# Performance work log

Measured on AMD Instinct MI355X. Metric: run time of the kernel, lower is better.

## Reference

```python
import jax, jax.numpy as jnp
import numpy as np

N = 50000      # number of graph nodes
D = 128        # in_dim == out_dim
R = 4          # num_ring
NNZ = 800000   # edges per ring (avg degree 16)


def setup_inputs() -> dict:
    key = jax.random.key(0)
    ks = jax.random.split(key, 12)
    s = 1.0 / np.sqrt(D)
    x = jax.random.normal(ks[0], (N, D), jnp.float32)
    W_self = jax.random.normal(ks[1], (D, D), jnp.float32) * s
    W_rings = jax.random.normal(ks[2], (R, D, D), jnp.float32) * s
    WC = jax.random.normal(ks[3], (D, D), jnp.float32) * s
    WD = jax.random.normal(ks[4], (D, D), jnp.float32) * s
    att_w = jax.random.normal(ks[5], (1, 2 * (R + 1) * D), jnp.float32) * s
    att_b = jnp.zeros((1,), jnp.float32)
    # degree^-0.5 style norms: positive, in (0, 1]
    out_deg_norm = jax.random.uniform(ks[6], (N, 1), jnp.float32, 0.05, 1.0)
    in_deg_norm = jax.random.uniform(ks[7], (N, 1), jnp.float32, 0.05, 1.0)
    rows = jax.random.randint(ks[8], (R, NNZ), 0, N, jnp.int32)
    cols = jax.random.randint(ks[9], (R, NNZ), 0, N, jnp.int32)
    return {"x": x, "W_self": W_self, "W_rings": W_rings, "WC": WC, "WD": WD,
            "att_w": att_w, "att_b": att_b, "out_deg_norm": out_deg_norm,
            "in_deg_norm": in_deg_norm, "rows": rows, "cols": cols}


def reference(x, W_self, W_rings, WC, WD, att_w, att_b, out_deg_norm, in_deg_norm, rows, cols):
    n, d = x.shape
    r = W_rings.shape[0]
    # ---- ring-wise sparse aggregation (dropout is identity at inference) ----
    z_self = x @ W_self.T                       # [N, D]
    z_list = [z_self]
    for i in range(r):
        h = (x @ W_rings[i].T) * out_deg_norm   # [N, D]
        # torch.sparse.mm(adj, h): out[row] += h[col] for each edge (row, col)
        z_i = jax.ops.segment_sum(h[cols[i]], rows[i], num_segments=n)
        z_list.append(z_i)
    z = jnp.concatenate(z_list, axis=1) * in_deg_norm   # [N, (R+1)*D]
    # ---- heterogeneous sensitivity interaction ----
    z3 = z.reshape(n, r + 1, d)                          # [N, R+1, D]
    z_hat_com = z3 @ WC                                  # [N, R+1, D]
    com_score = jnp.einsum('nrd,nsd->nrs', z_hat_com, z_hat_com)
    alpha_com = jax.nn.softmax(com_score, axis=-1)
    z_com = jnp.einsum('nrs,nsd->nrd', alpha_com, z_hat_com).reshape(n, -1)
    z_hat_dis = z3 @ WD                                  # [N, R+1, D]
    # pairwise differences: sub[n, r, s, :] = zd[n, r] - zd[n, s]
    sub = z_hat_dis[:, :, None, :] - z_hat_dis[:, None, :, :]   # [N, R+1, R+1, D]
    dis_score = jnp.einsum('nrd,nrsd->nrs', z_hat_dis, sub)
    alpha_dis = jax.nn.softmax(dis_score, axis=-1)
    z_dis = jnp.einsum('nrs,nrsd->nrd', alpha_dis, sub).reshape(n, -1)
    z_cat = jnp.concatenate([z_com, z_dis], axis=-1)     # [N, 2*(R+1)*D]
    beta = jax.nn.sigmoid(z_cat @ att_w.T + att_b)       # [N, 1]
    z_wave = beta * z_com + (1.0 - beta) * z_dis         # [N, (R+1)*D]
    return z_wave
```

## Files before the change

### kernel.cpp

```cpp
#include <hip/hip_runtime.h>
#include <hip/hip_bf16.h>

#define NN 50000
#define D 128
#define RR 4
#define NNZ 800000
#define NCHUNK 196

typedef float v2f    __attribute__((ext_vector_type(2)));
typedef float f32x4  __attribute__((ext_vector_type(4)));
typedef short bf16x8 __attribute__((ext_vector_type(8)));

static __device__ __forceinline__ unsigned short f2b(float f)
{
    __hip_bfloat16 h = __float2bfloat16(f);
    return *reinterpret_cast<unsigned short*>(&h);
}
static __device__ __forceinline__ float b2f(unsigned short u)
{
    union { unsigned u32; float f; } v; v.u32 = ((unsigned)u) << 16; return v.f;
}

__global__ __launch_bounds__(256) void hist_kernel(
    const int* __restrict__ rows, int* __restrict__ cnt)
{
    const int r = blockIdx.y;
    const int e = blockIdx.x * 256 + threadIdx.x;
    atomicAdd(&cnt[r * NN + rows[(size_t)r * NNZ + e]], 1);
}

__global__ __launch_bounds__(256) void scanA_kernel(
    const int* __restrict__ cnt, int* __restrict__ bsum)
{
    const int r = blockIdx.y, bx = blockIdx.x, t = threadIdx.x;
    const int idx = bx * 256 + t;
    int v = (idx < NN) ? cnt[r * NN + idx] : 0;
#pragma unroll
    for (int off = 32; off; off >>= 1) v += __shfl_xor(v, off);
    __shared__ int ws4[4];
    if ((t & 63) == 0) ws4[t >> 6] = v;
    __syncthreads();
    if (t == 0) bsum[r * NCHUNK + bx] = ws4[0] + ws4[1] + ws4[2] + ws4[3];
}

__global__ __launch_bounds__(256) void scanB_kernel(int* __restrict__ bsum)
{
    __shared__ int s[256];
    const int t = threadIdx.x;
    for (int r = 0; r < RR; ++r) {
        int v = (t < NCHUNK) ? bsum[r * NCHUNK + t] : 0;
        s[t] = v;
        __syncthreads();
        for (int off = 1; off < 256; off <<= 1) {
            int u = (t >= off) ? s[t - off] : 0;
            __syncthreads();
            s[t] += u;
            __syncthreads();
        }
        if (t < NCHUNK) bsum[r * NCHUNK + t] = s[t] - v;
        __syncthreads();
    }
}

__global__ __launch_bounds__(256) void scanC_kernel(
    const int* __restrict__ cnt, const int* __restrict__ bsum,
    int* __restrict__ rowptr, int* __restrict__ cursor)
{
    const int r = blockIdx.y, bx = blockIdx.x, t = threadIdx.x;
    const int idx = bx * 256 + t;
    int v = (idx < NN) ? cnt[r * NN + idx] : 0;
    __shared__ int s[256];
    s[t] = v;
    __syncthreads();
    for (int off = 1; off < 256; off <<= 1) {
        int u = (t >= off) ? s[t - off] : 0;
        __syncthreads();
        s[t] += u;
        __syncthreads();
    }
    const int excl = bsum[r * NCHUNK + bx] + s[t] - v;
    if (idx <= NN) rowptr[r * (NN + 1) + idx] = excl;
    if (idx < NN)  cursor[r * NN + idx] = excl;
}

__global__ __launch_bounds__(256) void fill_kernel(
    const int* __restrict__ rows, const int* __restrict__ cols,
    int* __restrict__ cursor, int* __restrict__ perm)
{
    const int r = blockIdx.y;
    const int e = blockIdx.x * 256 + threadIdx.x;
    const int row = rows[(size_t)r * NNZ + e];
    const int pos = atomicAdd(&cursor[r * NN + row], 1);
    perm[(size_t)r * NNZ + pos] = cols[(size_t)r * NNZ + e];
}

__global__ __launch_bounds__(256) void convw_kernel(
    const float* __restrict__ Wself, const float* __restrict__ Wrings,
    unsigned short* __restrict__ wh, unsigned short* __restrict__ wl)
{
    int idx = blockIdx.x * 256 + threadIdx.x;
    int jg = idx >> 7, k = idx & 127;
    float f = (jg < 128) ? Wself[(size_t)jg * 128 + k]
                         : Wrings[(size_t)(jg - 128) * 128 + k];
    unsigned short hi = f2b(f);
    wh[idx] = hi;
    wl[idx] = f2b(f - b2f(hi));
}

__global__ __launch_bounds__(256) void convt_kernel(
    const float* __restrict__ WC, const float* __restrict__ WD,
    unsigned short* __restrict__ wct_h, unsigned short* __restrict__ wct_l,
    unsigned short* __restrict__ wdt_h, unsigned short* __restrict__ wdt_l)
{
    int idx = blockIdx.x * 256 + threadIdx.x;
    int kk = idx >> 7, col = idx & 127;
    float c = WC[idx];
    float d = WD[idx];
    unsigned short ch = f2b(c), dh = f2b(d);
    wct_h[col * 128 + kk] = ch;
    wct_l[col * 128 + kk] = f2b(c - b2f(ch));
    wdt_h[col * 128 + kk] = dh;
    wdt_l[col * 128 + kk] = f2b(d - b2f(dh));
}

__global__ __launch_bounds__(256) void gather2_kernel(
    const float* __restrict__ x, const float* __restrict__ odn,
    const int* __restrict__ rp, const int* __restrict__ pm,
    float* __restrict__ y, int r0)
{
    const int cr = blockIdx.y + r0;
    const int t = threadIdx.x;
    const int row = blockIdx.x * 4 + (t >> 6);
    const int l  = t & 63;
    const int h  = l >> 5;
    const int dq = l & 31;
    const int* rpr = rp + (size_t)cr * (NN + 1);
    const int s = rpr[row], e = rpr[row + 1];
    const int* pmr = pm + (size_t)cr * NNZ;

    f32x4 acc = {0.f, 0.f, 0.f, 0.f};
    int i = s;
    for (; i + 8 <= e; i += 8) {
        int c0 = pmr[i + h],     c1 = pmr[i + 2 + h];
        int c2 = pmr[i + 4 + h], c3 = pmr[i + 6 + h];
        float o0 = odn[c0], o1 = odn[c1], o2 = odn[c2], o3 = odn[c3];
        f32x4 v0 = *(const f32x4*)&x[(size_t)c0 * D + dq * 4];
        f32x4 v1 = *(const f32x4*)&x[(size_t)c1 * D + dq * 4];
        f32x4 v2 = *(const f32x4*)&x[(size_t)c2 * D + dq * 4];
        f32x4 v3 = *(const f32x4*)&x[(size_t)c3 * D + dq * 4];
        acc += v0 * o0 + v1 * o1 + v2 * o2 + v3 * o3;
    }
    for (; i + h < e; i += 2) {
        int c = pmr[i + h];
        acc += (*(const f32x4*)&x[(size_t)c * D + dq * 4]) * odn[c];
    }
#pragma unroll
    for (int j = 0; j < 4; ++j) acc[j] += __shfl_xor(acc[j], 32);
    if (h == 0)
        *(f32x4*)&y[((size_t)blockIdx.y * NN + row) * D + dq * 4] = acc;
}

__global__ __launch_bounds__(256) void gemm5_kernel(
    const float* __restrict__ x, const float* __restrict__ y,
    const unsigned short* __restrict__ wh, const unsigned short* __restrict__ wl,
    float* __restrict__ out, int s0, int r0)
{
    const int s = s0 + blockIdx.y;
    const float* A = (s == 0) ? x : y + (size_t)(s - 1 - r0) * NN * D;
    const int t = threadIdx.x;
    const int w = t >> 6, l = t & 63;
    const int lr = l & 15, lk = l >> 4;
    const int n0 = blockIdx.x * 16;

    bf16x8 ah[4], al[4];
    const float* xr = A + (size_t)(n0 + lr) * D + lk * 8;
#pragma unroll
    for (int ks = 0; ks < 4; ++ks) {
        float4 v0 = *(const float4*)(xr + ks * 32);
        float4 v1 = *(const float4*)(xr + ks * 32 + 4);
        float f[8] = {v0.x, v0.y, v0.z, v0.w, v1.x, v1.y, v1.z, v1.w};
#pragma unroll
        for (int j = 0; j < 8; ++j) {
            unsigned short hi = f2b(f[j]);
            ah[ks][j] = (short)hi;
            al[ks][j] = (short)f2b(f[j] - b2f(hi));
        }
    }

#pragma unroll
    for (int j = 0; j < 2; ++j) {
        const int ctl = w + 4 * j;
        const int jg  = s * 128 + ctl * 16 + lr;
        f32x4 acc = {0.f, 0.f, 0.f, 0.f};
#pragma unroll
        for (int ks = 0; ks < 4; ++ks) {
            bf16x8 bhv = *(const bf16x8*)&wh[(size_t)jg * D + ks * 32 + lk * 8];
            bf16x8 blv = *(const bf16x8*)&wl[(size_t)jg * D + ks * 32 + lk * 8];
            acc = __builtin_amdgcn_mfma_f32_16x16x32_bf16(ah[ks], bhv, acc, 0, 0, 0);
            acc = __builtin_amdgcn_mfma_f32_16x16x32_bf16(al[ks], bhv, acc, 0, 0, 0);
            acc = __builtin_amdgcn_mfma_f32_16x16x32_bf16(ah[ks], blv, acc, 0, 0, 0);
        }
#pragma unroll
        for (int q = 0; q < 4; ++q) {
            int n = n0 + lk * 4 + q;
            out[(size_t)n * 640 + jg] = acc[q];
        }
    }
}

__device__ __forceinline__ int sidx(int r, int s)
{
    if (r > s) { int t = r; r = s; s = t; }
    return r * 5 + s - (r * (r + 1)) / 2;
}

__global__ __launch_bounds__(512, 4) void interact2_kernel(
    float* __restrict__ z,
    const unsigned short* __restrict__ wct_h, const unsigned short* __restrict__ wct_l,
    const unsigned short* __restrict__ wdt_h, const unsigned short* __restrict__ wdt_l,
    const float* __restrict__ att_w, const float* __restrict__ att_b,
    const float* __restrict__ idn)
{
    __shared__ float SB[2 * 5 * 16 * 128];

    const int t  = threadIdx.x;
    const int w  = t >> 6;
    const int l  = t & 63;
    const int lr = l & 15;
    const int lk = l >> 4;
    const int n0 = blockIdx.x * 16;

    const int mm = w >> 2;
    const int nq = w & 3;
    const unsigned short* bhp = mm ? wdt_h : wct_h;
    const unsigned short* blp = mm ? wdt_l : wct_l;

    f32x4 acc[5][2];
#pragma unroll
    for (int mt = 0; mt < 5; ++mt) {
        acc[mt][0] = (f32x4){0.f, 0.f, 0.f, 0.f};
        acc[mt][1] = (f32x4){0.f, 0.f, 0.f, 0.f};
    }

#pragma unroll
    for (int mt = 0; mt < 5; ++mt) {
        bf16x8 ah[4], al[4];
        const float* ap = z + (size_t)(n0 + lr) * 640 + mt * 128 + lk * 8;
#pragma unroll
        for (int ks = 0; ks < 4; ++ks) {
            float4 v0 = *(const float4*)(ap + ks * 32);
            float4 v1 = *(const float4*)(ap + ks * 32 + 4);
            float f[8] = {v0.x, v0.y, v0.z, v0.w, v1.x, v1.y, v1.z, v1.w};
#pragma unroll
            for (int j = 0; j < 8; ++j) {
                unsigned short hi = f2b(f[j]);
                ah[ks][j] = (short)hi;
                al[ks][j] = (short)f2b(f[j] - b2f(hi));
            }
        }
#pragma unroll
        for (int nt = 0; nt < 2; ++nt) {
            const int col = nq * 32 + nt * 16 + lr;
#pragma unroll
            for (int ks = 0; ks < 4; ++ks) {
                bf16x8 vh = *(const bf16x8*)&bhp[(size_t)col * 128 + ks * 32 + lk * 8];
                bf16x8 vl = *(const bf16x8*)&blp[(size_t)col * 128 + ks * 32 + lk * 8];
                acc[mt][nt] = __builtin_amdgcn_mfma_f32_16x16x32_bf16(ah[ks], vh, acc[mt][nt], 0, 0, 0);
                acc[mt][nt] = __builtin_amdgcn_mfma_f32_16x16x32_bf16(al[ks], vh, acc[mt][nt], 0, 0, 0);
                acc[mt][nt] = __builtin_amdgcn_mfma_f32_16x16x32_bf16(ah[ks], vl, acc[mt][nt], 0, 0, 0);
            }
        }
    }

#pragma unroll
    for (int mt = 0; mt < 5; ++mt)
#pragma unroll
        for (int nt = 0; nt < 2; ++nt) {
            const int col = nq * 32 + nt * 16 + lr;
#pragma unroll
            for (int q = 0; q < 4; ++q) {
                const int nd = lk * 4 + q;
                SB[(((mm * 5 + mt) * 16) + nd) * 128 + col] = acc[mt][nt][q];
            }
        }
    __syncthreads();

#pragma unroll
    for (int ii = 0; ii < 2; ++ii) {
        const int nd = w + ii * 8;
        const int n  = n0 + nd;
        const float nf = idn[n];

        v2f ar[5], dr[5];
#pragma unroll
        for (int r = 0; r < 5; ++r) {
            ar[r] = *(const v2f*)&SB[((r * 16) + nd) * 128 + 2 * l] * nf;
            dr[r] = *(const v2f*)&SB[(((5 + r) * 16) + nd) * 128 + 2 * l] * nf;
        }

        float pc[15], pd[15];
        {
            int k = 0;
#pragma unroll
            for (int r = 0; r < 5; ++r)
#pragma unroll
                for (int s = r; s < 5; ++s, ++k) {
                    v2f qc = ar[r] * ar[s];
                    v2f qd = dr[r] * dr[s];
                    float vc = qc.x + qc.y;
                    float vd = qd.x + qd.y;
#pragma unroll
                    for (int off = 32; off; off >>= 1) {
                        vc += __shfl_xor(vc, off);
                        vd += __shfl_xor(vd, off);
                    }
                    pc[k] = vc; pd[k] = vd;
                }
        }

        v2f zcom[5], zdis[5];
#pragma unroll
        for (int r = 0; r < 5; ++r) {
            float sc[5], m = -1e30f;
#pragma unroll
            for (int s = 0; s < 5; ++s) { sc[s] = pc[sidx(r, s)]; m = fmaxf(m, sc[s]); }
            float e[5], se = 0.f;
#pragma unroll
            for (int s = 0; s < 5; ++s) { e[s] = __expf(sc[s] - m); se += e[s]; }
            float inv = 1.f / se;
            v2f a2 = (v2f)0.f;
#pragma unroll
            for (int s = 0; s < 5; ++s) a2 += ar[s] * e[s];
            zcom[r] = a2 * inv;

            float qq = pd[sidx(r, r)];
            float sd[5], md = -1e30f;
#pragma unroll
            for (int s = 0; s < 5; ++s) { sd[s] = qq - pd[sidx(r, s)]; md = fmaxf(md, sd[s]); }
            float ed[5], sed = 0.f;
#pragma unroll
            for (int s = 0; s < 5; ++s) { ed[s] = __expf(sd[s] - md); sed += ed[s]; }
            float invd = 1.f / sed;
            v2f d2 = (v2f)0.f;
#pragma unroll
            for (int s = 0; s < 5; ++s) d2 += dr[s] * ed[s];
            zdis[r] = dr[r] - d2 * invd;
        }

        v2f p2 = (v2f)0.f;
#pragma unroll
        for (int r = 0; r < 5; ++r) {
            p2 += (*(const v2f*)&att_w[r * 128 + 2 * l]) * zcom[r];
            p2 += (*(const v2f*)&att_w[640 + r * 128 + 2 * l]) * zdis[r];
        }
        float part = p2.x + p2.y;
#pragma unroll
        for (int off = 32; off; off >>= 1) part += __shfl_xor(part, off);
        const float beta = 1.f / (1.f + __expf(-(part + att_b[0])));
        const float omb  = 1.f - beta;

#pragma unroll
        for (int r = 0; r < 5; ++r) {
            v2f o = zcom[r] * beta + zdis[r] * omb;
            *(v2f*)&z[(size_t)n * 640 + r * 128 + 2 * l] = o;
        }
    }
}

extern "C" void kernel_launch(void* const* d_in, const int* in_sizes, int n_in,
                              void* d_out, int out_size, void* d_ws, size_t ws_size,
                              hipStream_t stream)
{
    const float* x      = (const float*)d_in[0];
    const float* W_self = (const float*)d_in[1];
    const float* W_ring = (const float*)d_in[2];
    const float* WC     = (const float*)d_in[3];
    const float* WD     = (const float*)d_in[4];
    const float* att_w  = (const float*)d_in[5];
    const float* att_b  = (const float*)d_in[6];
    const float* odn    = (const float*)d_in[7];
    const float* idn    = (const float*)d_in[8];
    const int*   rows   = (const int*)d_in[9];
    const int*   cols   = (const int*)d_in[10];
    float* out = (float*)d_out;

    const size_t wb_sz  = (size_t)640 * 128 * 2;
    const size_t wt_sz  = (size_t)128 * 128 * 2;
    const size_t y1_sz  = (size_t)NN * D * 4;
    const size_t cnt_sz = (size_t)RR * NN * 4;
    const size_t rp_sz  = (size_t)RR * (NN + 1) * 4;
    const size_t cur_sz = (size_t)RR * NN * 4;
    const size_t bs_sz  = 4096;
    const size_t pm_sz  = (size_t)RR * NNZ * 4;
    const size_t fixed  = 2 * wb_sz + 4 * wt_sz + cnt_sz + rp_sz + cur_sz + bs_sz + pm_sz;
    const bool big = ws_size >= fixed + RR * y1_sz + 4096;

    char* p = (char*)d_ws;
    unsigned short* wh    = (unsigned short*)p; p += wb_sz;
    unsigned short* wl    = (unsigned short*)p; p += wb_sz;
    unsigned short* wct_h = (unsigned short*)p; p += wt_sz;
    unsigned short* wct_l = (unsigned short*)p; p += wt_sz;
    unsigned short* wdt_h = (unsigned short*)p; p += wt_sz;
    unsigned short* wdt_l = (unsigned short*)p; p += wt_sz;
    float* y    = (float*)p; p += (big ? RR : 1) * y1_sz;
    int* cnt    = (int*)p; p += cnt_sz;
    int* rowptr = (int*)p; p += rp_sz;
    int* cursor = (int*)p; p += cur_sz;
    int* bsum   = (int*)p; p += bs_sz;
    int* perm   = (int*)p;

    convw_kernel<<<320, 256, 0, stream>>>(W_self, W_ring, wh, wl);
    convt_kernel<<<64, 256, 0, stream>>>(WC, WD, wct_h, wct_l, wdt_h, wdt_l);

    hipMemsetAsync(cnt, 0, cnt_sz, stream);
    hist_kernel<<<dim3(NNZ / 256, RR), 256, 0, stream>>>(rows, cnt);
    scanA_kernel<<<dim3(NCHUNK, RR), 256, 0, stream>>>(cnt, bsum);
    scanB_kernel<<<1, 256, 0, stream>>>(bsum);
    scanC_kernel<<<dim3(NCHUNK, RR), 256, 0, stream>>>(cnt, bsum, rowptr, cursor);
    fill_kernel<<<dim3(NNZ / 256, RR), 256, 0, stream>>>(rows, cols, cursor, perm);

    if (big) {
        gather2_kernel<<<dim3(NN / 4, RR), 256, 0, stream>>>(x, odn, rowptr, perm, y, 0);
        gemm5_kernel<<<dim3(NN / 16, 5), 256, 0, stream>>>(x, y, wh, wl, out, 0, 0);
    } else {
        gemm5_kernel<<<dim3(NN / 16, 1), 256, 0, stream>>>(x, y, wh, wl, out, 0, 0);
        for (int r = 0; r < RR; ++r) {
            gather2_kernel<<<dim3(NN / 4, 1), 256, 0, stream>>>(x, odn, rowptr, perm, y, r);
            gemm5_kernel<<<dim3(NN / 16, 1), 256, 0, stream>>>(x, y, wh, wl, out, r + 1, r);
        }
    }

    interact2_kernel<<<NN / 16, 512, 0, stream>>>(out, wct_h, wct_l, wdt_h, wdt_l,
                                                  att_w, att_b, idn);
}
```

Baseline: 1.176 ms.

## Fuse per-ring projection GEMM with interaction kernel to skip z round-trip

In the big-workspace path, the 5-way projection GEMM and the interaction kernel are merged into one kernel. Each block computes its 16 nodes' z tile in registers, stages it as bf16 hi/lo in an 80KB LDS buffer, runs the WC/WD GEMMs and the softmax interaction from LDS, and writes only the final output. This removes writing and re-reading the N×640 fp32 intermediate and one kernel launch. In exchange, the large LDS footprint with 512 threads may limit occupancy, and the z values are re-split into bf16 hi/lo pairs rather than read from fp32.

```diff
diff --git a/kernel.cpp b/kernel.cpp
--- a/kernel.cpp
+++ b/kernel.cpp
@@ -212,6 +212,223 @@
 {
     if (r > s) { int t = r; r = s; s = t; }
     return r * 5 + s - (r * (r + 1)) / 2;
+}
+
+__global__ __launch_bounds__(512, 4) void fused_kernel(
+    const float* __restrict__ x, const float* __restrict__ y,
+    const unsigned short* __restrict__ wh, const unsigned short* __restrict__ wl,
+    const unsigned short* __restrict__ wct_h, const unsigned short* __restrict__ wct_l,
+    const unsigned short* __restrict__ wdt_h, const unsigned short* __restrict__ wdt_l,
+    const float* __restrict__ att_w, const float* __restrict__ att_b,
+    const float* __restrict__ idn, float* __restrict__ out)
+{
+    __shared__ __align__(16) char LB[81920];
+
+    const int t  = threadIdx.x;
+    const int w  = t >> 6;
+    const int l  = t & 63;
+    const int lr = l & 15;
+    const int lk = l >> 4;
+    const int n0 = blockIdx.x * 16;
+
+#pragma unroll
+    for (int i = 0; i < 5; ++i) {
+        const int fi = i * 512 + t;
+        const int e  = fi * 4;
+        const int s  = e >> 11;
+        const int nd = (e >> 7) & 15;
+        const int k0 = e & 127;
+        const float* src = (s == 0)
+            ? &x[(size_t)(n0 + nd) * 128 + k0]
+            : &y[((size_t)(s - 1) * NN + (n0 + nd)) * 128 + k0];
+        f32x4 v = *(const f32x4*)src;
+        const int row  = s * 16 + nd;
+        const int boff = ((row * 128 + k0) * 2) ^ ((row & 7) << 4);
+        ushort4 hv, lv;
+        unsigned short h0 = f2b(v[0]), h1 = f2b(v[1]), h2 = f2b(v[2]), h3 = f2b(v[3]);
+        hv.x = h0; hv.y = h1; hv.z = h2; hv.w = h3;
+        lv.x = f2b(v[0] - b2f(h0)); lv.y = f2b(v[1] - b2f(h1));
+        lv.z = f2b(v[2] - b2f(h2)); lv.w = f2b(v[3] - b2f(h3));
+        *(ushort4*)(LB + boff)         = hv;
+        *(ushort4*)(LB + 20480 + boff) = lv;
+    }
+    __syncthreads();
+
+    f32x4 zacc[5];
+#pragma unroll
+    for (int j = 0; j < 5; ++j) zacc[j] = (f32x4){0.f, 0.f, 0.f, 0.f};
+
+#pragma unroll
+    for (int j = 0; j < 5; ++j) {
+        const int jg = (w + 8 * j) * 16 + lr;
+#pragma unroll
+        for (int ks = 0; ks < 4; ++ks) {
+            const int arow  = j * 16 + lr;
+            const int abyte = ((arow * 128 + ks * 32 + lk * 8) * 2) ^ ((arow & 7) << 4);
+            bf16x8 ah = *(const bf16x8*)(LB + abyte);
+            bf16x8 al = *(const bf16x8*)(LB + 20480 + abyte);
+            bf16x8 bh = *(const bf16x8*)&wh[(size_t)jg * 128 + ks * 32 + lk * 8];
+            bf16x8 bl = *(const bf16x8*)&wl[(size_t)jg * 128 + ks * 32 + lk * 8];
+            zacc[j] = __builtin_amdgcn_mfma_f32_16x16x32_bf16(ah, bh, zacc[j], 0, 0, 0);
+            zacc[j] = __builtin_amdgcn_mfma_f32_16x16x32_bf16(al, bh, zacc[j], 0, 0, 0);
+            zacc[j] = __builtin_amdgcn_mfma_f32_16x16x32_bf16(ah, bl, zacc[j], 0, 0, 0);
+        }
+    }
+    __syncthreads();
+
+    {
+        const int k = w * 16 + lr;
+#pragma unroll
+        for (int j = 0; j < 5; ++j)
+#pragma unroll
+            for (int q = 0; q < 4; ++q) {
+                const int nd  = lk * 4 + q;
+                const int row = j * 16 + nd;
+                const float zv = zacc[j][q];
+                const unsigned short hi = f2b(zv);
+                const unsigned short lo = f2b(zv - b2f(hi));
+                const int boff = ((row * 128 + k) * 2) ^ ((row & 7) << 4);
+                *(unsigned short*)(LB + boff)         = hi;
+                *(unsigned short*)(LB + 20480 + boff) = lo;
+            }
+    }
+    __syncthreads();
+
+    const int mm = w >> 2;
+    const int nq = w & 3;
+    const unsigned short* bhp = mm ? wdt_h : wct_h;
+    const unsigned short* blp = mm ? wdt_l : wct_l;
+
+    f32x4 acc2[5][2];
+#pragma unroll
+    for (int mt = 0; mt < 5; ++mt) {
+        acc2[mt][0] = (f32x4){0.f, 0.f, 0.f, 0.f};
+        acc2[mt][1] = (f32x4){0.f, 0.f, 0.f, 0.f};
+    }
+
+#pragma unroll
+    for (int ks = 0; ks < 4; ++ks) {
+        const int c0 = nq * 32 + lr;
+        const int c1 = c0 + 16;
+        bf16x8 bh0 = *(const bf16x8*)&bhp[(size_t)c0 * 128 + ks * 32 + lk * 8];
+        bf16x8 bl0 = *(const bf16x8*)&blp[(size_t)c0 * 128 + ks * 32 + lk * 8];
+        bf16x8 bh1 = *(const bf16x8*)&bhp[(size_t)c1 * 128 + ks * 32 + lk * 8];
+        bf16x8 bl1 = *(const bf16x8*)&blp[(size_t)c1 * 128 + ks * 32 + lk * 8];
+#pragma unroll
+        for (int mt = 0; mt < 5; ++mt) {
+            const int arow  = mt * 16 + lr;
+            const int abyte = ((arow * 128 + ks * 32 + lk * 8) * 2) ^ ((arow & 7) << 4);
+            bf16x8 zh = *(const bf16x8*)(LB + abyte);
+            bf16x8 zl = *(const bf16x8*)(LB + 20480 + abyte);
+            acc2[mt][0] = __builtin_amdgcn_mfma_f32_16x16x32_bf16(zh, bh0, acc2[mt][0], 0, 0, 0);
+            acc2[mt][0] = __builtin_amdgcn_mfma_f32_16x16x32_bf16(zl, bh0, acc2[mt][0], 0, 0, 0);
+            acc2[mt][0] = __builtin_amdgcn_mfma_f32_16x16x32_bf16(zh, bl0, acc2[mt][0], 0, 0, 0);
+            acc2[mt][1] = __builtin_amdgcn_mfma_f32_16x16x32_bf16(zh, bh1, acc2[mt][1], 0, 0, 0);
+            acc2[mt][1] = __builtin_amdgcn_mfma_f32_16x16x32_bf16(zl, bh1, acc2[mt][1], 0, 0, 0);
+            acc2[mt][1] = __builtin_amdgcn_mfma_f32_16x16x32_bf16(zh, bl1, acc2[mt][1], 0, 0, 0);
+        }
+    }
+    __syncthreads();
+
+#pragma unroll
+    for (int mt = 0; mt < 5; ++mt)
+#pragma unroll
+        for (int nt = 0; nt < 2; ++nt) {
+            const int col = nq * 32 + nt * 16 + lr;
+#pragma unroll
+            for (int q = 0; q < 4; ++q) {
+                const int nd  = lk * 4 + q;
+                const int row = (mm * 5 + mt) * 16 + nd;
+                const int boff = (row * 512 + col * 4) ^ (((row >> 2) & 3) << 4);
+                *(float*)(LB + boff) = acc2[mt][nt][q];
+            }
+        }
+    __syncthreads();
+
+#pragma unroll
+    for (int ii = 0; ii < 2; ++ii) {
+        const int nd = w + ii * 8;
+        const int n  = n0 + nd;
+        const float nf = idn[n];
+
+        v2f ar[5], dr[5];
+#pragma unroll
+        for (int r = 0; r < 5; ++r) {
+            const int rowc = r * 16 + nd;
+            const int rowd = (5 + r) * 16 + nd;
+            const int bc = (rowc * 512 + l * 8) ^ (((rowc >> 2) & 3) << 4);
+            const int bd = (rowd * 512 + l * 8) ^ (((rowd >> 2) & 3) << 4);
+            ar[r] = *(const v2f*)(LB + bc) * nf;
+            dr[r] = *(const v2f*)(LB + bd) * nf;
+        }
+
+        float pc[15], pd[15];
+        {
+            int k = 0;
+#pragma unroll
+            for (int r = 0; r < 5; ++r)
+#pragma unroll
+                for (int s = r; s < 5; ++s, ++k) {
+                    v2f qc = ar[r] * ar[s];
+                    v2f qd = dr[r] * dr[s];
+                    float vc = qc.x + qc.y;
+                    float vd = qd.x + qd.y;
+#pragma unroll
+                    for (int off = 32; off; off >>= 1) {
+                        vc += __shfl_xor(vc, off);
+                        vd += __shfl_xor(vd, off);
+                    }
+                    pc[k] = vc; pd[k] = vd;
+                }
+        }
+
+        v2f zcom[5], zdis[5];
+#pragma unroll
+        for (int r = 0; r < 5; ++r) {
+            float sc[5], m = -1e30f;
+#pragma unroll
+            for (int s = 0; s < 5; ++s) { sc[s] = pc[sidx(r, s)]; m = fmaxf(m, sc[s]); }
+            float e[5], se = 0.f;
+#pragma unroll
+            for (int s = 0; s < 5; ++s) { e[s] = __expf(sc[s] - m); se += e[s]; }
+            float inv = 1.f / se;
+            v2f a2 = (v2f)0.f;
+#pragma unroll
+            for (int s = 0; s < 5; ++s) a2 += ar[s] * e[s];
+            zcom[r] = a2 * inv;
+
+            float qq = pd[sidx(r, r)];
+            float sd[5], md = -1e30f;
+#pragma unroll
+            for (int s = 0; s < 5; ++s) { sd[s] = qq - pd[sidx(r, s)]; md = fmaxf(md, sd[s]); }
+            float ed[5], sed = 0.f;
+#pragma unroll
+            for (int s = 0; s < 5; ++s) { ed[s] = __expf(sd[s] - md); sed += ed[s]; }
+            float invd = 1.f / sed;
+            v2f d2 = (v2f)0.f;
+#pragma unroll
+            for (int s = 0; s < 5; ++s) d2 += dr[s] * ed[s];
+            zdis[r] = dr[r] - d2 * invd;
+        }
+
+        v2f p2 = (v2f)0.f;
+#pragma unroll
+        for (int r = 0; r < 5; ++r) {
+            p2 += (*(const v2f*)&att_w[r * 128 + 2 * l]) * zcom[r];
+            p2 += (*(const v2f*)&att_w[640 + r * 128 + 2 * l]) * zdis[r];
+        }
+        float part = p2.x + p2.y;
+#pragma unroll
+        for (int off = 32; off; off >>= 1) part += __shfl_xor(part, off);
+        const float beta = 1.f / (1.f + __expf(-(part + att_b[0])));
+        const float omb  = 1.f - beta;
+
+#pragma unroll
+        for (int r = 0; r < 5; ++r) {
+            v2f o = zcom[r] * beta + zdis[r] * omb;
+            *(v2f*)&out[(size_t)n * 640 + r * 128 + 2 * l] = o;
+        }
+    }
 }
 
 __global__ __launch_bounds__(512, 4) void interact2_kernel(
@@ -421,15 +638,16 @@
 
     if (big) {
         gather2_kernel<<<dim3(NN / 4, RR), 256, 0, stream>>>(x, odn, rowptr, perm, y, 0);
-        gemm5_kernel<<<dim3(NN / 16, 5), 256, 0, stream>>>(x, y, wh, wl, out, 0, 0);
+        fused_kernel<<<NN / 16, 512, 0, stream>>>(x, y, wh, wl,
+                                                  wct_h, wct_l, wdt_h, wdt_l,
+                                                  att_w, att_b, idn, out);
     } else {
         gemm5_kernel<<<dim3(NN / 16, 1), 256, 0, stream>>>(x, y, wh, wl, out, 0, 0);
         for (int r = 0; r < RR; ++r) {
             gather2_kernel<<<dim3(NN / 4, 1), 256, 0, stream>>>(x, odn, rowptr, perm, y, r);
             gemm5_kernel<<<dim3(NN / 16, 1), 256, 0, stream>>>(x, y, wh, wl, out, r + 1, r);
         }
-    }
-
-    interact2_kernel<<<NN / 16, 512, 0, stream>>>(out, wct_h, wct_l, wdt_h, wdt_l,
-                                                  att_w, att_b, idn);
-}
+        interact2_kernel<<<NN / 16, 512, 0, stream>>>(out, wct_h, wct_l, wdt_h, wdt_l,
+                                                      att_w, att_b, idn);
+    }
+}
```

New measurement: 1.008 ms. 1.17x faster.

## Fold ring weights into WC/WD and fuse projection with interaction kernel

Applied to the files above, without the earlier changes.

Precomputes combined weight products (W_s^T·WC and W_s^T·WD) once, so the per-node pipeline does a single GEMM from the raw x and aggregated inputs straight into the com/dis projections. This removes the intermediate [N,640] z write/read and the separate gemm5 pass. Inputs are pre-split into bf16 hi/lo halves in global memory, the reductions use DPP/swizzle instead of shuffles, and shared memory gets an XOR swizzle. The fused kernel now does 10 matrix products per node tile and needs more workspace. The low-memory fallback path is dropped, and the reassociated weight product changes rounding slightly.

```diff
diff --git a/kernel.cpp b/kernel.cpp
--- a/kernel.cpp
+++ b/kernel.cpp
@@ -19,6 +19,21 @@
 static __device__ __forceinline__ float b2f(unsigned short u)
 {
     union { unsigned u32; float f; } v; v.u32 = ((unsigned)u) << 16; return v.f;
+}
+
+static __device__ __forceinline__ float redux32(float v)
+{
+    int i;
+    i = __builtin_amdgcn_update_dpp(0, __float_as_int(v), 0xB1, 0xF, 0xF, true);
+    v += __int_as_float(i);
+    i = __builtin_amdgcn_update_dpp(0, __float_as_int(v), 0x4E, 0xF, 0xF, true);
+    v += __int_as_float(i);
+    i = __builtin_amdgcn_update_dpp(0, __float_as_int(v), 0x141, 0xF, 0xF, true);
+    v += __int_as_float(i);
+    i = __builtin_amdgcn_update_dpp(0, __float_as_int(v), 0x140, 0xF, 0xF, true);
+    v += __int_as_float(i);
+    v += __int_as_float(__builtin_amdgcn_ds_swizzle(__float_as_int(v), 0x401F));
+    return v;
 }
 
 __global__ __launch_bounds__(256) void hist_kernel(
@@ -94,41 +109,51 @@
     perm[(size_t)r * NNZ + pos] = cols[(size_t)r * NNZ + e];
 }
 
-__global__ __launch_bounds__(256) void convw_kernel(
-    const float* __restrict__ Wself, const float* __restrict__ Wrings,
-    unsigned short* __restrict__ wh, unsigned short* __restrict__ wl)
-{
-    int idx = blockIdx.x * 256 + threadIdx.x;
-    int jg = idx >> 7, k = idx & 127;
-    float f = (jg < 128) ? Wself[(size_t)jg * 128 + k]
-                         : Wrings[(size_t)(jg - 128) * 128 + k];
-    unsigned short hi = f2b(f);
-    wh[idx] = hi;
-    wl[idx] = f2b(f - b2f(hi));
-}
-
-__global__ __launch_bounds__(256) void convt_kernel(
+__global__ __launch_bounds__(256) void convx_kernel(
+    const float* __restrict__ x,
+    unsigned short* __restrict__ xh, unsigned short* __restrict__ xl)
+{
+    const int i = blockIdx.x * 256 + threadIdx.x;
+    f32x4 v = ((const f32x4*)x)[i];
+    ushort4 hv, lv;
+#pragma unroll
+    for (int j = 0; j < 4; ++j) {
+        unsigned short hb = f2b(v[j]);
+        ((unsigned short*)&hv)[j] = hb;
+        ((unsigned short*)&lv)[j] = f2b(v[j] - b2f(hb));
+    }
+    ((ushort4*)xh)[i] = hv;
+    ((ushort4*)xl)[i] = lv;
+}
+
+__global__ __launch_bounds__(256) void convpt_kernel(
+    const float* __restrict__ Wself, const float* __restrict__ Wring,
     const float* __restrict__ WC, const float* __restrict__ WD,
-    unsigned short* __restrict__ wct_h, unsigned short* __restrict__ wct_l,
-    unsigned short* __restrict__ wdt_h, unsigned short* __restrict__ wdt_l)
-{
-    int idx = blockIdx.x * 256 + threadIdx.x;
-    int kk = idx >> 7, col = idx & 127;
-    float c = WC[idx];
-    float d = WD[idx];
-    unsigned short ch = f2b(c), dh = f2b(d);
-    wct_h[col * 128 + kk] = ch;
-    wct_l[col * 128 + kk] = f2b(c - b2f(ch));
-    wdt_h[col * 128 + kk] = dh;
-    wdt_l[col * 128 + kk] = f2b(d - b2f(dh));
+    unsigned short* __restrict__ PTh, unsigned short* __restrict__ PTl)
+{
+    const int idx = blockIdx.x * 256 + threadIdx.x;
+    const int m   = idx >> 14;
+    const int rem = idx & 16383;
+    const int col = rem >> 7;
+    const int kk  = rem & 127;
+    const float* WX = (m < 5) ? WC : WD;
+    const int s = (m < 5) ? m : m - 5;
+    const float* WS = (s == 0) ? Wself : Wring + (size_t)(s - 1) * 16384;
+    float acc = 0.f;
+#pragma unroll 4
+    for (int j = 0; j < 128; ++j)
+        acc += WX[j * 128 + col] * WS[j * 128 + kk];
+    unsigned short hb = f2b(acc);
+    PTh[idx] = hb;
+    PTl[idx] = f2b(acc - b2f(hb));
 }
 
 __global__ __launch_bounds__(256) void gather2_kernel(
     const float* __restrict__ x, const float* __restrict__ odn,
     const int* __restrict__ rp, const int* __restrict__ pm,
-    float* __restrict__ y, int r0)
-{
-    const int cr = blockIdx.y + r0;
+    unsigned short* __restrict__ yh, unsigned short* __restrict__ yl)
+{
+    const int cr = blockIdx.y;
     const int t = threadIdx.x;
     const int row = blockIdx.x * 4 + (t >> 6);
     const int l  = t & 63;
@@ -156,55 +181,18 @@
     }
 #pragma unroll
     for (int j = 0; j < 4; ++j) acc[j] += __shfl_xor(acc[j], 32);
-    if (h == 0)
-        *(f32x4*)&y[((size_t)blockIdx.y * NN + row) * D + dq * 4] = acc;
-}
-
-__global__ __launch_bounds__(256) void gemm5_kernel(
-    const float* __restrict__ x, const float* __restrict__ y,
-    const unsigned short* __restrict__ wh, const unsigned short* __restrict__ wl,
-    float* __restrict__ out, int s0, int r0)
-{
-    const int s = s0 + blockIdx.y;
-    const float* A = (s == 0) ? x : y + (size_t)(s - 1 - r0) * NN * D;
-    const int t = threadIdx.x;
-    const int w = t >> 6, l = t & 63;
-    const int lr = l & 15, lk = l >> 4;
-    const int n0 = blockIdx.x * 16;
-
-    bf16x8 ah[4], al[4];
-    const float* xr = A + (size_t)(n0 + lr) * D + lk * 8;
-#pragma unroll
-    for (int ks = 0; ks < 4; ++ks) {
-        float4 v0 = *(const float4*)(xr + ks * 32);
-        float4 v1 = *(const float4*)(xr + ks * 32 + 4);
-        float f[8] = {v0.x, v0.y, v0.z, v0.w, v1.x, v1.y, v1.z, v1.w};
-#pragma unroll
-        for (int j = 0; j < 8; ++j) {
-            unsigned short hi = f2b(f[j]);
-            ah[ks][j] = (short)hi;
-            al[ks][j] = (short)f2b(f[j] - b2f(hi));
+
+    if (h == 0) {
+        ushort4 hv, lv;
+#pragma unroll
+        for (int j = 0; j < 4; ++j) {
+            unsigned short hb = f2b(acc[j]);
+            ((unsigned short*)&hv)[j] = hb;
+            ((unsigned short*)&lv)[j] = f2b(acc[j] - b2f(hb));
         }
-    }
-
-#pragma unroll
-    for (int j = 0; j < 2; ++j) {
-        const int ctl = w + 4 * j;
-        const int jg  = s * 128 + ctl * 16 + lr;
-        f32x4 acc = {0.f, 0.f, 0.f, 0.f};
-#pragma unroll
-        for (int ks = 0; ks < 4; ++ks) {
-            bf16x8 bhv = *(const bf16x8*)&wh[(size_t)jg * D + ks * 32 + lk * 8];
-            bf16x8 blv = *(const bf16x8*)&wl[(size_t)jg * D + ks * 32 + lk * 8];
-            acc = __builtin_amdgcn_mfma_f32_16x16x32_bf16(ah[ks], bhv, acc, 0, 0, 0);
-            acc = __builtin_amdgcn_mfma_f32_16x16x32_bf16(al[ks], bhv, acc, 0, 0, 0);
-            acc = __builtin_amdgcn_mfma_f32_16x16x32_bf16(ah[ks], blv, acc, 0, 0, 0);
-        }
-#pragma unroll
-        for (int q = 0; q < 4; ++q) {
-            int n = n0 + lk * 4 + q;
-            out[(size_t)n * 640 + jg] = acc[q];
-        }
+        const size_t base = ((size_t)cr * NN + row) * D + dq * 4;
+        *(ushort4*)&yh[base] = hv;
+        *(ushort4*)&yl[base] = lv;
     }
 }
 
@@ -214,14 +202,19 @@
     return r * 5 + s - (r * (r + 1)) / 2;
 }
 
-__global__ __launch_bounds__(512, 4) void interact2_kernel(
-    float* __restrict__ z,
-    const unsigned short* __restrict__ wct_h, const unsigned short* __restrict__ wct_l,
-    const unsigned short* __restrict__ wdt_h, const unsigned short* __restrict__ wdt_l,
+__device__ __forceinline__ int sboff(int m, int node, int col)
+{
+    return (((m * 16 + node) * 128 + col) * 4) ^ ((node & 7) << 4);
+}
+
+__global__ __launch_bounds__(512, 4) void fused2_kernel(
+    const unsigned short* __restrict__ xh, const unsigned short* __restrict__ xl,
+    const unsigned short* __restrict__ yh, const unsigned short* __restrict__ yl,
+    const unsigned short* __restrict__ PTh, const unsigned short* __restrict__ PTl,
     const float* __restrict__ att_w, const float* __restrict__ att_b,
-    const float* __restrict__ idn)
-{
-    __shared__ float SB[2 * 5 * 16 * 128];
+    const float* __restrict__ idn, float* __restrict__ out)
+{
+    __shared__ __align__(16) char LB[81920];
 
     const int t  = threadIdx.x;
     const int w  = t >> 6;
@@ -230,140 +223,115 @@
     const int lk = l >> 4;
     const int n0 = blockIdx.x * 16;
 
-    const int mm = w >> 2;
-    const int nq = w & 3;
-    const unsigned short* bhp = mm ? wdt_h : wct_h;
-    const unsigned short* blp = mm ? wdt_l : wct_l;
-
-    f32x4 acc[5][2];
-#pragma unroll
-    for (int mt = 0; mt < 5; ++mt) {
-        acc[mt][0] = (f32x4){0.f, 0.f, 0.f, 0.f};
-        acc[mt][1] = (f32x4){0.f, 0.f, 0.f, 0.f};
-    }
-
-#pragma unroll
-    for (int mt = 0; mt < 5; ++mt) {
-        bf16x8 ah[4], al[4];
-        const float* ap = z + (size_t)(n0 + lr) * 640 + mt * 128 + lk * 8;
+    f32x4 acc[10];
+#pragma unroll
+    for (int m = 0; m < 10; ++m) acc[m] = (f32x4){0.f, 0.f, 0.f, 0.f};
+
+#pragma unroll
+    for (int s = 0; s < 5; ++s) {
+        const unsigned short* bhq = (s == 0 ? xh : yh + (size_t)(s - 1) * NN * D)
+                                    + (size_t)(n0 + lr) * D + lk * 8;
+        const unsigned short* blq = (s == 0 ? xl : yl + (size_t)(s - 1) * NN * D)
+                                    + (size_t)(n0 + lr) * D + lk * 8;
+        const int arow = (w * 16 + lr) * 128 + lk * 8;
+        const unsigned short* a0h = PTh + (size_t)s * 16384 + arow;
+        const unsigned short* a0l = PTl + (size_t)s * 16384 + arow;
+        const unsigned short* a1h = PTh + (size_t)(5 + s) * 16384 + arow;
+        const unsigned short* a1l = PTl + (size_t)(5 + s) * 16384 + arow;
 #pragma unroll
         for (int ks = 0; ks < 4; ++ks) {
-            float4 v0 = *(const float4*)(ap + ks * 32);
-            float4 v1 = *(const float4*)(ap + ks * 32 + 4);
-            float f[8] = {v0.x, v0.y, v0.z, v0.w, v1.x, v1.y, v1.z, v1.w};
-#pragma unroll
-            for (int j = 0; j < 8; ++j) {
-                unsigned short hi = f2b(f[j]);
-                ah[ks][j] = (short)hi;
-                al[ks][j] = (short)f2b(f[j] - b2f(hi));
+            bf16x8 bh  = *(const bf16x8*)(bhq + ks * 32);
+            bf16x8 bl  = *(const bf16x8*)(blq + ks * 32);
+            bf16x8 ah0 = *(const bf16x8*)(a0h + ks * 32);
+            bf16x8 al0 = *(const bf16x8*)(a0l + ks * 32);
+            bf16x8 ah1 = *(const bf16x8*)(a1h + ks * 32);
+            bf16x8 al1 = *(const bf16x8*)(a1l + ks * 32);
+            acc[s] = __builtin_amdgcn_mfma_f32_16x16x32_bf16(ah0, bh, acc[s], 0, 0, 0);
+            acc[s] = __builtin_amdgcn_mfma_f32_16x16x32_bf16(al0, bh, acc[s], 0, 0, 0);
+            acc[s] = __builtin_amdgcn_mfma_f32_16x16x32_bf16(ah0, bl, acc[s], 0, 0, 0);
+            acc[5 + s] = __builtin_amdgcn_mfma_f32_16x16x32_bf16(ah1, bh, acc[5 + s], 0, 0, 0);
+            acc[5 + s] = __builtin_amdgcn_mfma_f32_16x16x32_bf16(al1, bh, acc[5 + s], 0, 0, 0);
+            acc[5 + s] = __builtin_amdgcn_mfma_f32_16x16x32_bf16(ah1, bl, acc[5 + s], 0, 0, 0);
+        }
+    }
+
+#pragma unroll
+    for (int m = 0; m < 10; ++m)
+        *(f32x4*)(LB + sboff(m, lr, w * 16 + lk * 4)) = acc[m];
+    __syncthreads();
+
+    const int lg = l & 31;
+    const int nd = w * 2 + (l >> 5);
+    const int n  = n0 + nd;
+    const float nf = idn[n];
+
+    f32x4 ar[5], dr[5];
+#pragma unroll
+    for (int r = 0; r < 5; ++r) {
+        ar[r] = *(const f32x4*)(LB + sboff(r, nd, lg * 4)) * nf;
+        dr[r] = *(const f32x4*)(LB + sboff(5 + r, nd, lg * 4)) * nf;
+    }
+
+    float pc[15], pd[15];
+    {
+        int k = 0;
+#pragma unroll
+        for (int r = 0; r < 5; ++r)
+#pragma unroll
+            for (int s = r; s < 5; ++s, ++k) {
+                f32x4 qc = ar[r] * ar[s];
+                f32x4 qd = dr[r] * dr[s];
+                pc[k] = redux32((qc[0] + qc[1]) + (qc[2] + qc[3]));
+                pd[k] = redux32((qd[0] + qd[1]) + (qd[2] + qd[3]));
             }
-        }
-#pragma unroll
-        for (int nt = 0; nt < 2; ++nt) {
-            const int col = nq * 32 + nt * 16 + lr;
-#pragma unroll
-            for (int ks = 0; ks < 4; ++ks) {
-                bf16x8 vh = *(const bf16x8*)&bhp[(size_t)col * 128 + ks * 32 + lk * 8];
-                bf16x8 vl = *(const bf16x8*)&blp[(size_t)col * 128 + ks * 32 + lk * 8];
-                acc[mt][nt] = __builtin_amdgcn_mfma_f32_16x16x32_bf16(ah[ks], vh, acc[mt][nt], 0, 0, 0);
-                acc[mt][nt] = __builtin_amdgcn_mfma_f32_16x16x32_bf16(al[ks], vh, acc[mt][nt], 0, 0, 0);
-                acc[mt][nt] = __builtin_amdgcn_mfma_f32_16x16x32_bf16(ah[ks], vl, acc[mt][nt], 0, 0, 0);
-            }
-        }
-    }
-
-#pragma unroll
-    for (int mt = 0; mt < 5; ++mt)
-#pragma unroll
-        for (int nt = 0; nt < 2; ++nt) {
-            const int col = nq * 32 + nt * 16 + lr;
-#pragma unroll
-            for (int q = 0; q < 4; ++q) {
-                const int nd = lk * 4 + q;
-                SB[(((mm * 5 + mt) * 16) + nd) * 128 + col] = acc[mt][nt][q];
-            }
-        }
-    __syncthreads();
-
-#pragma unroll
-    for (int ii = 0; ii < 2; ++ii) {
-        const int nd = w + ii * 8;
-        const int n  = n0 + nd;
-        const float nf = idn[n];
-
-        v2f ar[5], dr[5];
-#pragma unroll
-        for (int r = 0; r < 5; ++r) {
-            ar[r] = *(const v2f*)&SB[((r * 16) + nd) * 128 + 2 * l] * nf;
-            dr[r] = *(const v2f*)&SB[(((5 + r) * 16) + nd) * 128 + 2 * l] * nf;
-        }
-
-        float pc[15], pd[15];
-        {
-            int k = 0;
-#pragma unroll
-            for (int r = 0; r < 5; ++r)
-#pragma unroll
-                for (int s = r; s < 5; ++s, ++k) {
-                    v2f qc = ar[r] * ar[s];
-                    v2f qd = dr[r] * dr[s];
-                    float vc = qc.x + qc.y;
-                    float vd = qd.x + qd.y;
-#pragma unroll
-                    for (int off = 32; off; off >>= 1) {
-                        vc += __shfl_xor(vc, off);
-                        vd += __shfl_xor(vd, off);
-                    }
-                    pc[k] = vc; pd[k] = vd;
-                }
-        }
-
-        v2f zcom[5], zdis[5];
-#pragma unroll
-        for (int r = 0; r < 5; ++r) {
-            float sc[5], m = -1e30f;
-#pragma unroll
-            for (int s = 0; s < 5; ++s) { sc[s] = pc[sidx(r, s)]; m = fmaxf(m, sc[s]); }
-            float e[5], se = 0.f;
-#pragma unroll
-            for (int s = 0; s < 5; ++s) { e[s] = __expf(sc[s] - m); se += e[s]; }
-            float inv = 1.f / se;
-            v2f a2 = (v2f)0.f;
-#pragma unroll
-            for (int s = 0; s < 5; ++s) a2 += ar[s] * e[s];
-            zcom[r] = a2 * inv;
-
-            float qq = pd[sidx(r, r)];
-            float sd[5], md = -1e30f;
-#pragma unroll
-            for (int s = 0; s < 5; ++s) { sd[s] = qq - pd[sidx(r, s)]; md = fmaxf(md, sd[s]); }
-            float ed[5], sed = 0.f;
-#pragma unroll
-            for (int s = 0; s < 5; ++s) { ed[s] = __expf(sd[s] - md); sed += ed[s]; }
-            float invd = 1.f / sed;
-            v2f d2 = (v2f)0.f;
-#pragma unroll
-            for (int s = 0; s < 5; ++s) d2 += dr[s] * ed[s];
-            zdis[r] = dr[r] - d2 * invd;
-        }
-
-        v2f p2 = (v2f)0.f;
-#pragma unroll
-        for (int r = 0; r < 5; ++r) {
-            p2 += (*(const v2f*)&att_w[r * 128 + 2 * l]) * zcom[r];
-            p2 += (*(const v2f*)&att_w[640 + r * 128 + 2 * l]) * zdis[r];
-        }
-        float part = p2.x + p2.y;
-#pragma unroll
-        for (int off = 32; off; off >>= 1) part += __shfl_xor(part, off);
-        const float beta = 1.f / (1.f + __expf(-(part + att_b[0])));
-        const float omb  = 1.f - beta;
-
-#pragma unroll
-        for (int r = 0; r < 5; ++r) {
-            v2f o = zcom[r] * beta + zdis[r] * omb;
-            *(v2f*)&z[(size_t)n * 640 + r * 128 + 2 * l] = o;
-        }
+    }
+
+    f32x4 zcom[5];
+#pragma unroll
+    for (int r = 0; r < 5; ++r) {
+        float sc[5], m = -1e30f;
+#pragma unroll
+        for (int s = 0; s < 5; ++s) { sc[s] = pc[sidx(r, s)]; m = fmaxf(m, sc[s]); }
+        float e[5], se = 0.f;
+#pragma unroll
+        for (int s = 0; s < 5; ++s) { e[s] = __expf(sc[s] - m); se += e[s]; }
+        float inv = 1.f / se;
+        f32x4 a2 = (f32x4){0.f, 0.f, 0.f, 0.f};
+#pragma unroll
+        for (int s = 0; s < 5; ++s) a2 += ar[s] * e[s];
+        zcom[r] = a2 * inv;
+    }
+    f32x4 zdis[5];
+#pragma unroll
+    for (int r = 0; r < 5; ++r) {
+        float qq = pd[sidx(r, r)];
+        float sd[5], md = -1e30f;
+#pragma unroll
+        for (int s = 0; s < 5; ++s) { sd[s] = qq - pd[sidx(r, s)]; md = fmaxf(md, sd[s]); }
+        float ed[5], sed = 0.f;
+#pragma unroll
+        for (int s = 0; s < 5; ++s) { ed[s] = __expf(sd[s] - md); sed += ed[s]; }
+        float invd = 1.f / sed;
+        f32x4 d2 = (f32x4){0.f, 0.f, 0.f, 0.f};
+#pragma unroll
+        for (int s = 0; s < 5; ++s) d2 += dr[s] * ed[s];
+        zdis[r] = dr[r] - d2 * invd;
+    }
+
+    f32x4 p4 = (f32x4){0.f, 0.f, 0.f, 0.f};
+#pragma unroll
+    for (int r = 0; r < 5; ++r) {
+        p4 += (*(const f32x4*)&att_w[r * 128 + lg * 4]) * zcom[r];
+        p4 += (*(const f32x4*)&att_w[640 + r * 128 + lg * 4]) * zdis[r];
+    }
+    float part = redux32((p4[0] + p4[1]) + (p4[2] + p4[3]));
+    const float beta = 1.f / (1.f + __expf(-(part + att_b[0])));
+    const float omb  = 1.f - beta;
+
+#pragma unroll
+    for (int r = 0; r < 5; ++r) {
+        f32x4 o = zcom[r] * beta + zdis[r] * omb;
+        *(f32x4*)&out[(size_t)n * 640 + r * 128 + lg * 4] = o;
     }
 }
 
@@ -384,33 +352,29 @@
     const int*   cols   = (const int*)d_in[10];
     float* out = (float*)d_out;
 
-    const size_t wb_sz  = (size_t)640 * 128 * 2;
-    const size_t wt_sz  = (size_t)128 * 128 * 2;
-    const size_t y1_sz  = (size_t)NN * D * 4;
+    const size_t xs_sz  = (size_t)NN * D * 2;
+    const size_t ys_sz  = (size_t)RR * NN * D * 2;
+    const size_t pt_sz  = (size_t)10 * 128 * 128 * 2;
     const size_t cnt_sz = (size_t)RR * NN * 4;
     const size_t rp_sz  = (size_t)RR * (NN + 1) * 4;
     const size_t cur_sz = (size_t)RR * NN * 4;
     const size_t bs_sz  = 4096;
-    const size_t pm_sz  = (size_t)RR * NNZ * 4;
-    const size_t fixed  = 2 * wb_sz + 4 * wt_sz + cnt_sz + rp_sz + cur_sz + bs_sz + pm_sz;
-    const bool big = ws_size >= fixed + RR * y1_sz + 4096;
 
     char* p = (char*)d_ws;
-    unsigned short* wh    = (unsigned short*)p; p += wb_sz;
-    unsigned short* wl    = (unsigned short*)p; p += wb_sz;
-    unsigned short* wct_h = (unsigned short*)p; p += wt_sz;
-    unsigned short* wct_l = (unsigned short*)p; p += wt_sz;
-    unsigned short* wdt_h = (unsigned short*)p; p += wt_sz;
-    unsigned short* wdt_l = (unsigned short*)p; p += wt_sz;
-    float* y    = (float*)p; p += (big ? RR : 1) * y1_sz;
+    unsigned short* xh  = (unsigned short*)p; p += xs_sz;
+    unsigned short* xl  = (unsigned short*)p; p += xs_sz;
+    unsigned short* yh  = (unsigned short*)p; p += ys_sz;
+    unsigned short* yl  = (unsigned short*)p; p += ys_sz;
+    unsigned short* PTh = (unsigned short*)p; p += pt_sz;
+    unsigned short* PTl = (unsigned short*)p; p += pt_sz;
     int* cnt    = (int*)p; p += cnt_sz;
     int* rowptr = (int*)p; p += rp_sz;
     int* cursor = (int*)p; p += cur_sz;
     int* bsum   = (int*)p; p += bs_sz;
     int* perm   = (int*)p;
 
-    convw_kernel<<<320, 256, 0, stream>>>(W_self, W_ring, wh, wl);
-    convt_kernel<<<64, 256, 0, stream>>>(WC, WD, wct_h, wct_l, wdt_h, wdt_l);
+    convx_kernel<<<6250, 256, 0, stream>>>(x, xh, xl);
+    convpt_kernel<<<640, 256, 0, stream>>>(W_self, W_ring, WC, WD, PTh, PTl);
 
     hipMemsetAsync(cnt, 0, cnt_sz, stream);
     hist_kernel<<<dim3(NNZ / 256, RR), 256, 0, stream>>>(rows, cnt);
@@ -419,17 +383,8 @@
     scanC_kernel<<<dim3(NCHUNK, RR), 256, 0, stream>>>(cnt, bsum, rowptr, cursor);
     fill_kernel<<<dim3(NNZ / 256, RR), 256, 0, stream>>>(rows, cols, cursor, perm);
 
-    if (big) {
-        gather2_kernel<<<dim3(NN / 4, RR), 256, 0, stream>>>(x, odn, rowptr, perm, y, 0);
-        gemm5_kernel<<<dim3(NN / 16, 5), 256, 0, stream>>>(x, y, wh, wl, out, 0, 0);
-    } else {
-        gemm5_kernel<<<dim3(NN / 16, 1), 256, 0, stream>>>(x, y, wh, wl, out, 0, 0);
-        for (int r = 0; r < RR; ++r) {
-            gather2_kernel<<<dim3(NN / 4, 1), 256, 0, stream>>>(x, odn, rowptr, perm, y, r);
-            gemm5_kernel<<<dim3(NN / 16, 1), 256, 0, stream>>>(x, y, wh, wl, out, r + 1, r);
-        }
-    }
-
-    interact2_kernel<<<NN / 16, 512, 0, stream>>>(out, wct_h, wct_l, wdt_h, wdt_l,
-                                                  att_w, att_b, idn);
-}
+    gather2_kernel<<<dim3(NN / 4, RR), 256, 0, stream>>>(x, odn, rowptr, perm, yh, yl);
+
+    fused2_kernel<<<NN / 16, 512, 0, stream>>>(xh, xl, yh, yl, PTh, PTl,
+                                               att_w, att_b, idn, out);
+}
```

New measurement: 1.144 ms. 2.7% less time.
